# Optimization experiments

Measured on AMD Instinct MI355X. Metric: run time of the kernel, lower is better.

The kernel has to match this reference:

```python
import jax, jax.numpy as jnp
import numpy as np

NEG_SLOPE = 0.2  # PyG GATConv default negative_slope


def gat_conv(x, src, dst, W, a_src, a_dst, b, n_nodes):
    # x: [N, Cin]; W: [H, Cin, Cout]; a_src/a_dst: [H, Cout]; b: [Cout]
    xh = jnp.einsum('ni,hio->nho', x, W)                 # [N, H, Cout]
    al_s = jnp.einsum('nho,ho->nh', xh, a_src)           # [N, H]
    al_d = jnp.einsum('nho,ho->nh', xh, a_dst)           # [N, H]
    e = jax.nn.leaky_relu(al_s[src] + al_d[dst], NEG_SLOPE)  # [E, H]
    # softmax over incoming edges of each dst node (self-loops guarantee >=1 edge)
    m = jax.ops.segment_max(e, dst, num_segments=n_nodes)
    ex = jnp.exp(e - m[dst])
    den = jax.ops.segment_sum(ex, dst, num_segments=n_nodes)
    alpha = ex / den[dst]                                # [E, H]
    msg = alpha[:, :, None] * xh[src]                    # [E, H, Cout]
    out = jax.ops.segment_sum(msg, dst, num_segments=n_nodes)  # [N, H, Cout]
    return out.mean(axis=1) + b                          # concat=False -> head mean


def setup_inputs() -> dict:
    key = jax.random.key(0)
    ks = jax.random.split(key, 16)
    N, E, C, H = 20000, 320000, 128, 4
    s = 1.0 / np.sqrt(C)
    inp = {
        'x': jax.random.normal(ks[0], (N, C), dtype=jnp.float32),
        'edge_index': jax.random.randint(ks[1], (2, E), 0, N, dtype=jnp.int64),
    }
    for i, name in enumerate(['1', '2', 'r']):
        k0, k1, k2 = jax.random.split(ks[2 + i], 3)
        inp['W' + name] = jax.random.normal(k0, (H, C, C), dtype=jnp.float32) * s
        inp['as' + name] = jax.random.normal(k1, (H, C), dtype=jnp.float32) * s
        inp['ad' + name] = jax.random.normal(k2, (H, C), dtype=jnp.float32) * s
        inp['b' + name] = jnp.zeros((C,), dtype=jnp.float32)
    return inp


def reference(x, edge_index, W1, as1, ad1, b1, W2, as2, ad2, b2, Wr, asr, adr, br):
    n = x.shape[0]
    loop = jnp.arange(n, dtype=edge_index.dtype)
    src = jnp.concatenate([edge_index[0], loop])  # PyG add_self_loops=True
    dst = jnp.concatenate([edge_index[1], loop])
    h = gat_conv(x, src, dst, W1, as1, ad1, b1, n)
    h = gat_conv(h, src, dst, W2, as2, ad2, b2, n)
    res = gat_conv(x, src, dst, Wr, asr, adr, br, n)
    return h + res
```

## Files before the change

kernel.cpp:

```cpp
#include <hip/hip_runtime.h>
#include <math.h>

#define C 128

typedef unsigned short u16;
typedef __attribute__((ext_vector_type(8))) short short8;
typedef __attribute__((ext_vector_type(4))) float f32x4;
typedef __attribute__((ext_vector_type(4))) u16 u16x4;

__device__ __forceinline__ float b2f(u16 u) {
    union { unsigned i; float f; } x; x.i = (unsigned)u << 16; return x.f;
}
__device__ __forceinline__ u16 f2b(float f) {
    union { float f; unsigned i; } x; x.f = f;
    unsigned r = x.i + 0x7FFFu + ((x.i >> 16) & 1u);
    return (u16)(r >> 16);
}
__device__ __forceinline__ float lrelu(float x) { return x > 0.f ? x : 0.2f * x; }


__global__ void hist_kernel(const int* __restrict__ ei, int E, int N,
                            int* __restrict__ count) {
    int total = E + N;
    for (int e = blockIdx.x * blockDim.x + threadIdx.x; e < total;
         e += gridDim.x * blockDim.x) {
        int d = (e < E) ? ei[E + e] : (e - E);
        if ((unsigned)d < (unsigned)N) atomicAdd(&count[d], 1);
    }
}

__global__ __launch_bounds__(1024) void scan_kernel(const int* __restrict__ count,
                                                    int* __restrict__ offs,
                                                    int* __restrict__ cursor, int N) {
    int tid = threadIdx.x, lane = tid & 63, wid = tid >> 6;
    int CH = (N + 1023) >> 10;
    int base = tid * CH;
    int s = 0;
    for (int j = 0; j < CH; ++j) {
        int i = base + j;
        if (i < N) s += count[i];
    }
    int own = s;
    #pragma unroll
    for (int d = 1; d < 64; d <<= 1) {
        int v = __shfl_up(s, d);
        if (lane >= d) s += v;
    }
    __shared__ int wtot[16];
    if (lane == 63) wtot[wid] = s;
    __syncthreads();
    if (tid < 16) {
        int t = wtot[tid];
        int u = t;
        #pragma unroll
        for (int d = 1; d < 16; d <<= 1) {
            int v = __shfl_up(u, d);
            if (tid >= d) u += v;
        }
        wtot[tid] = u - t;
        if (tid == 15) offs[N] = u;
    }
    __syncthreads();
    int run = wtot[wid] + s - own;
    for (int j = 0; j < CH; ++j) {
        int i = base + j;
        if (i < N) {
            offs[i] = run;
            cursor[i] = run;
            run += count[i];
        }
    }
}

__global__ void scatter_kernel(const int* __restrict__ ei, int E, int N,
                               int* __restrict__ cursor, int* __restrict__ srcs,
                               int* __restrict__ dsts) {
    int total = E + N;
    for (int e = blockIdx.x * blockDim.x + threadIdx.x; e < total;
         e += gridDim.x * blockDim.x) {
        int sNode, d;
        if (e < E) { sNode = ei[e]; d = ei[E + e]; }
        else       { sNode = e - E; d = sNode; }
        if ((unsigned)d < (unsigned)N && (unsigned)sNode < (unsigned)N) {
            int pos = atomicAdd(&cursor[d], 1);
            srcs[pos] = sNode;
            dsts[pos] = d;
        }
    }
}

__global__ __launch_bounds__(128) void cvt_w_kernel(const float* __restrict__ W1,
                                                    const float* __restrict__ Wr,
                                                    const float* __restrict__ W2,
                                                    u16* __restrict__ Wc) {
    int b = blockIdx.x;
    int l = b >> 7, o = b & 127;
    const float* W = (l == 0) ? W1 : (l == 1) ? Wr : W2;
    int i = threadIdx.x;
    u16* dst = Wc + ((size_t)l * C + o) * 512;
    #pragma unroll
    for (int h = 0; h < 4; ++h) {
        dst[h * C + i] = f2b(0.25f * W[((size_t)h * C + i) * C + o]);
    }
}


__global__ __launch_bounds__(256) void wvec_kernel(const float* __restrict__ W1,
                                                   const float* __restrict__ as1,
                                                   const float* __restrict__ ad1,
                                                   const float* __restrict__ Wr,
                                                   const float* __restrict__ asr,
                                                   const float* __restrict__ adr,
                                                   const float* __restrict__ W2,
                                                   const float* __restrict__ as2,
                                                   const float* __restrict__ ad2,
                                                   u16* __restrict__ vsdA,
                                                   u16* __restrict__ vsdB) {
    int slot = blockIdx.x;
    const float* W  = (slot < 4) ? W1 : (slot < 8) ? Wr : W2;
    const float* s_ = (slot < 4) ? as1 : (slot < 8) ? asr : as2;
    const float* d_ = (slot < 4) ? ad1 : (slot < 8) ? adr : ad2;
    int h = slot & 3;
    int wave = threadIdx.x >> 6, lane = threadIdx.x & 63;
    int rbase = blockIdx.y * 32 + wave * 8;
    float as0 = s_[h * C + lane], as1v = s_[h * C + 64 + lane];
    float ad0 = d_[h * C + lane], ad1v = d_[h * C + 64 + lane];
    #pragma unroll
    for (int j = 0; j < 8; ++j) {
        int i = rbase + j;
        const float* Wrow = W + ((size_t)h * C + i) * C;
        float w0 = Wrow[lane], w1 = Wrow[64 + lane];
        float ps = w0 * as0 + w1 * as1v;
        float pd = w0 * ad0 + w1 * ad1v;
        #pragma unroll
        for (int m = 32; m; m >>= 1) {
            ps += __shfl_xor(ps, m);
            pd += __shfl_xor(pd, m);
        }
        if (lane == 0) {
            if (slot < 8) {
                vsdA[slot * C + i] = f2b(ps);
                vsdA[(8 + slot) * C + i] = f2b(pd);
            } else {
                vsdB[(slot - 8) * C + i] = f2b(ps);
                vsdB[(4 + (slot - 8)) * C + i] = f2b(pd);
            }
        }
    }
}


__global__ __launch_bounds__(256) void alA_kernel(const float* __restrict__ x,
                                                  const u16* __restrict__ vsd,
                                                  u16* __restrict__ xb,
                                                  float* __restrict__ als,
                                                  float* __restrict__ ald, int N) {
    int wave = threadIdx.x >> 6, lane = threadIdx.x & 63;
    int rowBase = blockIdx.x * 64 + wave * 16;
    int r = rowBase + (lane & 15);
    int rl = r < N ? r : N - 1;
    int kg = (lane >> 4) * 8;

    short8 a[4];
    #pragma unroll
    for (int t = 0; t < 4; ++t) {
        const float* xp = x + (size_t)rl * C + t * 32 + kg;
        float4 f0 = *(const float4*)xp;
        float4 f1 = *(const float4*)(xp + 4);
        short8 s;
        s[0] = f2b(f0.x); s[1] = f2b(f0.y); s[2] = f2b(f0.z); s[3] = f2b(f0.w);
        s[4] = f2b(f1.x); s[5] = f2b(f1.y); s[6] = f2b(f1.z); s[7] = f2b(f1.w);
        a[t] = s;
        if (r < N) *(short8*)(xb + (size_t)r * C + t * 32 + kg) = s;
    }
    f32x4 acc = {0.f, 0.f, 0.f, 0.f};
    int col = lane & 15;
    #pragma unroll
    for (int t = 0; t < 4; ++t) {
        short8 b = *(const short8*)(vsd + (size_t)col * C + t * 32 + kg);
        acc = __builtin_amdgcn_mfma_f32_16x16x32_bf16(a[t], b, acc, 0, 0, 0);
    }
    #pragma unroll
    for (int j = 0; j < 4; ++j) {
        int rr = rowBase + (lane >> 4) * 4 + j;
        if (rr < N) {
            if (col < 8) als[rr * 8 + col] = acc[j];
            else ald[rr * 8 + (col - 8)] = acc[j];
        }
    }
}


__global__ __launch_bounds__(256) void alB_kernel(const u16* __restrict__ in,
                                                  const u16* __restrict__ vsd,
                                                  float* __restrict__ als,
                                                  float* __restrict__ ald, int N) {
    int wave = threadIdx.x >> 6, lane = threadIdx.x & 63;
    int rowBase = blockIdx.x * 64 + wave * 16;
    int r = rowBase + (lane & 15);
    int rl = r < N ? r : N - 1;
    int kg = (lane >> 4) * 8;

    f32x4 acc = {0.f, 0.f, 0.f, 0.f};
    int col = lane & 15;
    #pragma unroll
    for (int t = 0; t < 4; ++t) {
        short8 a = *(const short8*)(in + (size_t)rl * C + t * 32 + kg);
        short8 b = *(const short8*)(vsd + (size_t)col * C + t * 32 + kg);
        acc = __builtin_amdgcn_mfma_f32_16x16x32_bf16(a, b, acc, 0, 0, 0);
    }
    #pragma unroll
    for (int j = 0; j < 4; ++j) {
        int rr = rowBase + (lane >> 4) * 4 + j;
        if (rr < N && col < 8) {
            if (col < 4) als[rr * 4 + col] = acc[j];
            else ald[rr * 4 + (col - 4)] = acc[j];
        }
    }
}


template <int NH>
__global__ __launch_bounds__(256) void ew_kernel(const float* __restrict__ als,
                                                 const float* __restrict__ ald,
                                                 const int* __restrict__ srcs,
                                                 const int* __restrict__ dsts,
                                                 float* __restrict__ wout, int ET) {
    int i = blockIdx.x * blockDim.x + threadIdx.x;
    if (i >= ET) return;
    int s = srcs[i], d = dsts[i];
    const float* as_ = als + (size_t)s * NH;
    const float* ad_ = ald + (size_t)d * NH;
    float* wo = wout + (size_t)i * NH;
    #pragma unroll
    for (int h = 0; h < NH; ++h) {
        wo[h] = __expf(lrelu(as_[h] + ad_[h]));
    }
}


template <int NH>
__global__ __launch_bounds__(256) void den_kernel(const float* __restrict__ wgt,
                                                  const int* __restrict__ offs,
                                                  float* __restrict__ den, int N) {
    int idx = blockIdx.x * blockDim.x + threadIdx.x;
    int node = idx / NH, h = idx % NH;
    if (node >= N) return;
    int beg = offs[node], end = offs[node + 1];
    float s = 0.f;
    for (int i = beg; i < end; ++i) s += wgt[(size_t)i * NH + h];
    den[idx] = s;
}


template <int NH>
__global__ __launch_bounds__(256) void aggx_kernel(const u16* __restrict__ xsrc,
                                                   const float* __restrict__ wgt,
                                                   const float* __restrict__ den,
                                                   const int* __restrict__ offs,
                                                   const int* __restrict__ srcs,
                                                   u16* __restrict__ dest, int N) {
    constexpr int NHG = NH / 2;
    int node = blockIdx.x * 4 + (threadIdx.x >> 6);
    int lane = threadIdx.x & 63;
    if (node >= N) return;
    int g = lane >> 5;
    int c0 = (lane & 31) * 4;
    int beg = offs[node], end = offs[node + 1];

    float inv[NHG];
    #pragma unroll
    for (int j = 0; j < NHG; ++j) {
        inv[j] = 1.f / den[(size_t)node * NH + g * NHG + j];
    }

    float acc[NHG][4] = {};
    int i = beg;
    for (; i + 8 <= end; i += 8) {
        int s[8];
        #pragma unroll
        for (int e = 0; e < 8; ++e) s[e] = srcs[i + e];
        u16x4 v[8];
        #pragma unroll
        for (int e = 0; e < 8; ++e) {
            v[e] = *(const u16x4*)(xsrc + (size_t)s[e] * C + c0);
        }
        float wv[8][NHG];
        #pragma unroll
        for (int e = 0; e < 8; ++e) {
            if constexpr (NHG == 4) {
                float4 wq = *(const float4*)(wgt + (size_t)(i + e) * NH + g * NHG);
                wv[e][0] = wq.x; wv[e][1] = wq.y; wv[e][2] = wq.z; wv[e][3] = wq.w;
            } else {
                float2 wq = *(const float2*)(wgt + (size_t)(i + e) * NH + g * NHG);
                wv[e][0] = wq.x; wv[e][1] = wq.y;
            }
        }
        #pragma unroll
        for (int e = 0; e < 8; ++e) {
            float f[4];
            #pragma unroll
            for (int j = 0; j < 4; ++j) f[j] = b2f(v[e][j]);
            #pragma unroll
            for (int j2 = 0; j2 < NHG; ++j2) {
                #pragma unroll
                for (int j = 0; j < 4; ++j) acc[j2][j] += wv[e][j2] * f[j];
            }
        }
    }
    for (; i < end; ++i) {
        int s0 = srcs[i];
        u16x4 v0 = *(const u16x4*)(xsrc + (size_t)s0 * C + c0);
        float w0[NHG];
        #pragma unroll
        for (int j2 = 0; j2 < NHG; ++j2) {
            w0[j2] = wgt[(size_t)i * NH + g * NHG + j2];
        }
        float f[4];
        #pragma unroll
        for (int j = 0; j < 4; ++j) f[j] = b2f(v0[j]);
        #pragma unroll
        for (int j2 = 0; j2 < NHG; ++j2) {
            #pragma unroll
            for (int j = 0; j < 4; ++j) acc[j2][j] += w0[j2] * f[j];
        }
    }

    #pragma unroll
    for (int j2 = 0; j2 < NHG; ++j2) {
        int h = g * NHG + j2;
        u16x4 o = {f2b(acc[j2][0] * inv[j2]), f2b(acc[j2][1] * inv[j2]),
                   f2b(acc[j2][2] * inv[j2]), f2b(acc[j2][3] * inv[j2])};
        *(u16x4*)(dest + (size_t)node * (NH * C) + h * C + c0) = o;
    }
}


__global__ __launch_bounds__(256) void gemm2ab_kernel(const u16* __restrict__ agg,
                                                      const u16* __restrict__ Wc,
                                                      const float* __restrict__ b1,
                                                      const float* __restrict__ br,
                                                      u16* __restrict__ h1b,
                                                      float* __restrict__ outf, int N) {
    int part = blockIdx.y;
    const u16* A = agg + part * 512;
    const u16* W = Wc + (size_t)part * C * 512;
    const float* bias = part ? br : b1;

    int wave = threadIdx.x >> 6, lane = threadIdx.x & 63;
    int rowBase = blockIdx.x * 64 + wave * 16;
    int r = rowBase + (lane & 15);
    int rl = r < N ? r : N - 1;
    int kg = (lane >> 4) * 8;

    const short8* ap = (const short8*)(A + (size_t)rl * 1024 + kg);
    const short8* bp = (const short8*)(W + (size_t)(lane & 15) * 512 + kg);

    f32x4 acc[8];
    #pragma unroll
    for (int t = 0; t < 8; ++t) acc[t] = (f32x4){0.f, 0.f, 0.f, 0.f};

    #pragma unroll
    for (int kk = 0; kk < 16; ++kk) {
        short8 a = ap[kk * 4];
        #pragma unroll
        for (int t = 0; t < 8; ++t) {
            acc[t] = __builtin_amdgcn_mfma_f32_16x16x32_bf16(
                a, bp[(size_t)t * 16 * 64 + kk * 4], acc[t], 0, 0, 0);
        }
    }

    int prow = rowBase + (lane >> 4) * 4;
    #pragma unroll
    for (int t = 0; t < 8; ++t) {
        int col = t * 16 + (lane & 15);
        float bcol = bias[col];
        #pragma unroll
        for (int j = 0; j < 4; ++j) {
            int rr = prow + j;
            if (rr < N) {
                float v = acc[t][j] + bcol;
                if (part == 0) h1b[(size_t)rr * C + col] = f2b(v);
                else outf[(size_t)rr * C + col] = v;
            }
        }
    }
}


__global__ __launch_bounds__(256) void gemm2c_kernel(const u16* __restrict__ A,
                                                     const u16* __restrict__ Wc,
                                                     const float* __restrict__ bias,
                                                     float* __restrict__ outf, int N) {
    int wave = threadIdx.x >> 6, lane = threadIdx.x & 63;
    int rowBase = blockIdx.x * 64 + wave * 16;
    int r = rowBase + (lane & 15);
    int rl = r < N ? r : N - 1;
    int kg = (lane >> 4) * 8;

    const short8* ap = (const short8*)(A + (size_t)rl * 512 + kg);
    const short8* bp = (const short8*)(Wc + (size_t)(lane & 15) * 512 + kg);

    f32x4 acc[8];
    #pragma unroll
    for (int t = 0; t < 8; ++t) acc[t] = (f32x4){0.f, 0.f, 0.f, 0.f};

    #pragma unroll
    for (int kk = 0; kk < 16; ++kk) {
        short8 a = ap[kk * 4];
        #pragma unroll
        for (int t = 0; t < 8; ++t) {
            acc[t] = __builtin_amdgcn_mfma_f32_16x16x32_bf16(
                a, bp[(size_t)t * 16 * 64 + kk * 4], acc[t], 0, 0, 0);
        }
    }

    int prow = rowBase + (lane >> 4) * 4;
    #pragma unroll
    for (int t = 0; t < 8; ++t) {
        int col = t * 16 + (lane & 15);
        float bcol = bias[col];
        #pragma unroll
        for (int j = 0; j < 4; ++j) {
            int rr = prow + j;
            if (rr < N) outf[(size_t)rr * C + col] += acc[t][j] + bcol;
        }
    }
}


extern "C" void kernel_launch(void* const* d_in, const int* in_sizes, int n_in,
                              void* d_out, int out_size, void* d_ws, size_t ws_size,
                              hipStream_t stream) {
    const float* x = (const float*)d_in[0];
    const int* ei = (const int*)d_in[1];
    const float* W1 = (const float*)d_in[2];
    const float* as1 = (const float*)d_in[3];
    const float* ad1 = (const float*)d_in[4];
    const float* b1 = (const float*)d_in[5];
    const float* W2 = (const float*)d_in[6];
    const float* as2 = (const float*)d_in[7];
    const float* ad2 = (const float*)d_in[8];
    const float* b2 = (const float*)d_in[9];
    const float* Wr = (const float*)d_in[10];
    const float* asr = (const float*)d_in[11];
    const float* adr = (const float*)d_in[12];
    const float* br = (const float*)d_in[13];

    int N = in_sizes[0] / C;
    int E = in_sizes[1] / 2;
    int ET = E + N;

    size_t sz_xb    = (size_t)N * C * 2;
    size_t sz_h1b   = (size_t)N * C * 2;
    size_t sz_aggA  = (size_t)N * 1024 * 2;
    size_t sz_aggB  = (size_t)N * 512 * 2;
    size_t sz_wc    = (size_t)3 * C * 512 * 2;
    size_t sz_vsd   = (size_t)16 * C * 2;
    size_t sz_al8   = (size_t)N * 8 * 4;
    size_t sz_count = (size_t)N * 4;
    size_t sz_den8  = (size_t)N * 8 * 4;
    size_t sz_den4  = (size_t)N * 4 * 4;
    size_t sz_offs  = (size_t)(N + 4) * 4;
    size_t sz_srcs  = (size_t)ET * 4;
    size_t sz_w     = (size_t)ET * 8 * 4;
    size_t required = sz_xb + sz_h1b + sz_aggA + sz_aggB + sz_wc + 2 * sz_vsd +
                      2 * sz_al8 + sz_count + sz_den8 + sz_den4 + sz_count +
                      sz_offs + 2 * sz_srcs + sz_w;
    if (ws_size < required) return;

    char* w = (char*)d_ws;
    u16* xb = (u16*)w;        w += sz_xb;
    u16* h1b = (u16*)w;       w += sz_h1b;
    u16* aggA = (u16*)w;      w += sz_aggA;
    u16* aggB = (u16*)w;      w += sz_aggB;
    u16* Wc = (u16*)w;        w += sz_wc;
    u16* vsdA = (u16*)w;      w += sz_vsd;
    u16* vsdB = (u16*)w;      w += sz_vsd;
    float* als = (float*)w;   w += sz_al8;
    float* ald = (float*)w;   w += sz_al8;
    int* count = (int*)w;     w += sz_count;
    float* den8 = (float*)w;  w += sz_den8;
    float* den4 = (float*)w;  w += sz_den4;
    int* cursor = (int*)w;    w += sz_count;
    int* offs = (int*)w;      w += sz_offs;
    int* srcs = (int*)w;      w += sz_srcs;
    int* dsts = (int*)w;      w += sz_srcs;
    float* wgt = (float*)w;   w += sz_w;
    float* out = (float*)d_out;

    const u16* Wc2 = Wc + (size_t)2 * C * 512;

    hipMemsetAsync(count, 0, sz_count, stream);
    hist_kernel<<<512, 256, 0, stream>>>(ei, E, N, count);
    scan_kernel<<<1, 1024, 0, stream>>>(count, offs, cursor, N);
    scatter_kernel<<<512, 256, 0, stream>>>(ei, E, N, cursor, srcs, dsts);

    cvt_w_kernel<<<384, 128, 0, stream>>>(W1, Wr, W2, Wc);
    wvec_kernel<<<dim3(12, 4), 256, 0, stream>>>(W1, as1, ad1, Wr, asr, adr,
                                                 W2, as2, ad2, vsdA, vsdB);

    int nwb = (N + 3) / 4;
    int neb = (ET + 255) / 256;
    int gx = (N + 63) / 64;
    int nd8 = (N * 8 + 255) / 256;
    int nd4 = (N * 4 + 255) / 256;

    alA_kernel<<<gx, 256, 0, stream>>>(x, vsdA, xb, als, ald, N);
    ew_kernel<8><<<neb, 256, 0, stream>>>(als, ald, srcs, dsts, wgt, ET);
    den_kernel<8><<<nd8, 256, 0, stream>>>(wgt, offs, den8, N);
    aggx_kernel<8><<<nwb, 256, 0, stream>>>(xb, wgt, den8, offs, srcs, aggA, N);
    gemm2ab_kernel<<<dim3(gx, 2), 256, 0, stream>>>(aggA, Wc, b1, br, h1b, out, N);

    alB_kernel<<<gx, 256, 0, stream>>>(h1b, vsdB, als, ald, N);
    ew_kernel<4><<<neb, 256, 0, stream>>>(als, ald, srcs, dsts, wgt, ET);
    den_kernel<4><<<nd4, 256, 0, stream>>>(wgt, offs, den4, N);
    aggx_kernel<4><<<nwb, 256, 0, stream>>>(h1b, wgt, den4, offs, srcs, aggB, N);
    gemm2c_kernel<<<gx, 256, 0, stream>>>(aggB, Wc2, b2, out, N);
}
```

Measured before the change: 375.8 us.

## Pre-swizzle bf16 weights into MFMA fragment order and double rows per wave

The weight-conversion kernel now writes bf16 weights already arranged in per-lane MFMA B-fragment order, so each lane loads its B operand as one contiguous 16-byte read that coalesces across the wave instead of a strided one. Both output GEMM kernels also process two 16-row tiles per wave (128 rows per block), reusing each loaded B fragment for two MFMAs. This halves weight traffic per row, at the cost of more accumulator registers and half as many blocks.

```diff
diff --git a/kernel.cpp b/kernel.cpp
--- a/kernel.cpp
+++ b/kernel.cpp
@@ -89,19 +89,27 @@
     }
 }
 
-__global__ __launch_bounds__(128) void cvt_w_kernel(const float* __restrict__ W1,
+
+__global__ __launch_bounds__(256) void cvt_w_kernel(const float* __restrict__ W1,
                                                     const float* __restrict__ Wr,
                                                     const float* __restrict__ W2,
-                                                    u16* __restrict__ Wc) {
-    int b = blockIdx.x;
-    int l = b >> 7, o = b & 127;
+                                                    u16* __restrict__ Wf) {
+    int idx = blockIdx.x * 256 + threadIdx.x;
+    int lane = idx & 63;
+    int kk = (idx >> 6) & 15;
+    int t = (idx >> 10) & 7;
+    int l = idx >> 13;
+    if (l >= 3) return;
     const float* W = (l == 0) ? W1 : (l == 1) ? Wr : W2;
-    int i = threadIdx.x;
-    u16* dst = Wc + ((size_t)l * C + o) * 512;
-    #pragma unroll
-    for (int h = 0; h < 4; ++h) {
-        dst[h * C + i] = f2b(0.25f * W[((size_t)h * C + i) * C + o]);
-    }
+    int o = t * 16 + (lane & 15);
+    int bk = kk * 32 + (lane >> 4) * 8;
+    int h = bk >> 7, i0 = bk & 127;
+    short8 v;
+    #pragma unroll
+    for (int j = 0; j < 8; ++j) {
+        v[j] = (short)f2b(0.25f * W[((size_t)h * C + i0 + j) * C + o]);
+    }
+    *(short8*)(Wf + (size_t)idx * 8) = v;
 }
 
 
@@ -337,93 +345,112 @@
 
 
 __global__ __launch_bounds__(256) void gemm2ab_kernel(const u16* __restrict__ agg,
-                                                      const u16* __restrict__ Wc,
+                                                      const u16* __restrict__ Wf,
                                                       const float* __restrict__ b1,
                                                       const float* __restrict__ br,
                                                       u16* __restrict__ h1b,
                                                       float* __restrict__ outf, int N) {
     int part = blockIdx.y;
-    const u16* A = agg + part * 512;
-    const u16* W = Wc + (size_t)part * C * 512;
     const float* bias = part ? br : b1;
-
     int wave = threadIdx.x >> 6, lane = threadIdx.x & 63;
-    int rowBase = blockIdx.x * 64 + wave * 16;
-    int r = rowBase + (lane & 15);
-    int rl = r < N ? r : N - 1;
-    int kg = (lane >> 4) * 8;
-
-    const short8* ap = (const short8*)(A + (size_t)rl * 1024 + kg);
-    const short8* bp = (const short8*)(W + (size_t)(lane & 15) * 512 + kg);
-
-    f32x4 acc[8];
-    #pragma unroll
-    for (int t = 0; t < 8; ++t) acc[t] = (f32x4){0.f, 0.f, 0.f, 0.f};
+    int rowBase = blockIdx.x * 128 + wave * 32;
+    int p = lane & 15, q = lane >> 4;
+    int r0 = rowBase + p, r1 = rowBase + 16 + p;
+    int rl0 = r0 < N ? r0 : N - 1;
+    int rl1 = r1 < N ? r1 : N - 1;
+    int kg = q * 8;
+
+    const short8* ap0 = (const short8*)(agg + (size_t)rl0 * 1024 + part * 512 + kg);
+    const short8* ap1 = (const short8*)(agg + (size_t)rl1 * 1024 + part * 512 + kg);
+    const u16* wb = Wf + (size_t)part * 65536 + lane * 8;
+
+    f32x4 acc0[8], acc1[8];
+    #pragma unroll
+    for (int t = 0; t < 8; ++t) {
+        acc0[t] = (f32x4){0.f, 0.f, 0.f, 0.f};
+        acc1[t] = (f32x4){0.f, 0.f, 0.f, 0.f};
+    }
 
     #pragma unroll
     for (int kk = 0; kk < 16; ++kk) {
-        short8 a = ap[kk * 4];
+        short8 a0 = ap0[kk * 4];
+        short8 a1 = ap1[kk * 4];
         #pragma unroll
         for (int t = 0; t < 8; ++t) {
-            acc[t] = __builtin_amdgcn_mfma_f32_16x16x32_bf16(
-                a, bp[(size_t)t * 16 * 64 + kk * 4], acc[t], 0, 0, 0);
-        }
-    }
-
-    int prow = rowBase + (lane >> 4) * 4;
+            short8 b = *(const short8*)(wb + (size_t)(t * 16 + kk) * 512);
+            acc0[t] = __builtin_amdgcn_mfma_f32_16x16x32_bf16(a0, b, acc0[t], 0, 0, 0);
+            acc1[t] = __builtin_amdgcn_mfma_f32_16x16x32_bf16(a1, b, acc1[t], 0, 0, 0);
+        }
+    }
+
     #pragma unroll
     for (int t = 0; t < 8; ++t) {
-        int col = t * 16 + (lane & 15);
+        int col = t * 16 + p;
         float bcol = bias[col];
         #pragma unroll
         for (int j = 0; j < 4; ++j) {
-            int rr = prow + j;
-            if (rr < N) {
-                float v = acc[t][j] + bcol;
-                if (part == 0) h1b[(size_t)rr * C + col] = f2b(v);
-                else outf[(size_t)rr * C + col] = v;
+            int rr0 = rowBase + q * 4 + j;
+            int rr1 = rowBase + 16 + q * 4 + j;
+            if (rr0 < N) {
+                float v = acc0[t][j] + bcol;
+                if (part == 0) h1b[(size_t)rr0 * C + col] = f2b(v);
+                else outf[(size_t)rr0 * C + col] = v;
             }
+            if (rr1 < N) {
+                float v = acc1[t][j] + bcol;
+                if (part == 0) h1b[(size_t)rr1 * C + col] = f2b(v);
+                else outf[(size_t)rr1 * C + col] = v;
+            }
         }
     }
 }
 
 
 __global__ __launch_bounds__(256) void gemm2c_kernel(const u16* __restrict__ A,
-                                                     const u16* __restrict__ Wc,
+                                                     const u16* __restrict__ Wf,
                                                      const float* __restrict__ bias,
                                                      float* __restrict__ outf, int N) {
     int wave = threadIdx.x >> 6, lane = threadIdx.x & 63;
-    int rowBase = blockIdx.x * 64 + wave * 16;
-    int r = rowBase + (lane & 15);
-    int rl = r < N ? r : N - 1;
-    int kg = (lane >> 4) * 8;
-
-    const short8* ap = (const short8*)(A + (size_t)rl * 512 + kg);
-    const short8* bp = (const short8*)(Wc + (size_t)(lane & 15) * 512 + kg);
-
-    f32x4 acc[8];
-    #pragma unroll
-    for (int t = 0; t < 8; ++t) acc[t] = (f32x4){0.f, 0.f, 0.f, 0.f};
+    int rowBase = blockIdx.x * 128 + wave * 32;
+    int p = lane & 15, q = lane >> 4;
+    int r0 = rowBase + p, r1 = rowBase + 16 + p;
+    int rl0 = r0 < N ? r0 : N - 1;
+    int rl1 = r1 < N ? r1 : N - 1;
+    int kg = q * 8;
+
+    const short8* ap0 = (const short8*)(A + (size_t)rl0 * 512 + kg);
+    const short8* ap1 = (const short8*)(A + (size_t)rl1 * 512 + kg);
+    const u16* wb = Wf + (size_t)2 * 65536 + lane * 8;
+
+    f32x4 acc0[8], acc1[8];
+    #pragma unroll
+    for (int t = 0; t < 8; ++t) {
+        acc0[t] = (f32x4){0.f, 0.f, 0.f, 0.f};
+        acc1[t] = (f32x4){0.f, 0.f, 0.f, 0.f};
+    }
 
     #pragma unroll
     for (int kk = 0; kk < 16; ++kk) {
-        short8 a = ap[kk * 4];
+        short8 a0 = ap0[kk * 4];
+        short8 a1 = ap1[kk * 4];
         #pragma unroll
         for (int t = 0; t < 8; ++t) {
-            acc[t] = __builtin_amdgcn_mfma_f32_16x16x32_bf16(
-                a, bp[(size_t)t * 16 * 64 + kk * 4], acc[t], 0, 0, 0);
-        }
-    }
-
-    int prow = rowBase + (lane >> 4) * 4;
+            short8 b = *(const short8*)(wb + (size_t)(t * 16 + kk) * 512);
+            acc0[t] = __builtin_amdgcn_mfma_f32_16x16x32_bf16(a0, b, acc0[t], 0, 0, 0);
+            acc1[t] = __builtin_amdgcn_mfma_f32_16x16x32_bf16(a1, b, acc1[t], 0, 0, 0);
+        }
+    }
+
     #pragma unroll
     for (int t = 0; t < 8; ++t) {
-        int col = t * 16 + (lane & 15);
+        int col = t * 16 + p;
         float bcol = bias[col];
         #pragma unroll
         for (int j = 0; j < 4; ++j) {
-            int rr = prow + j;
-            if (rr < N) outf[(size_t)rr * C + col] += acc[t][j] + bcol;
+            int rr0 = rowBase + q * 4 + j;
+            int rr1 = rowBase + 16 + q * 4 + j;
+            if (rr0 < N) outf[(size_t)rr0 * C + col] += acc0[t][j] + bcol;
+            if (rr1 < N) outf[(size_t)rr1 * C + col] += acc1[t][j] + bcol;
         }
     }
 }
@@ -474,7 +501,7 @@
     u16* h1b = (u16*)w;       w += sz_h1b;
     u16* aggA = (u16*)w;      w += sz_aggA;
     u16* aggB = (u16*)w;      w += sz_aggB;
-    u16* Wc = (u16*)w;        w += sz_wc;
+    u16* Wf = (u16*)w;        w += sz_wc;
     u16* vsdA = (u16*)w;      w += sz_vsd;
     u16* vsdB = (u16*)w;      w += sz_vsd;
     float* als = (float*)w;   w += sz_al8;
@@ -489,20 +516,19 @@
     float* wgt = (float*)w;   w += sz_w;
     float* out = (float*)d_out;
 
-    const u16* Wc2 = Wc + (size_t)2 * C * 512;
-
     hipMemsetAsync(count, 0, sz_count, stream);
     hist_kernel<<<512, 256, 0, stream>>>(ei, E, N, count);
     scan_kernel<<<1, 1024, 0, stream>>>(count, offs, cursor, N);
     scatter_kernel<<<512, 256, 0, stream>>>(ei, E, N, cursor, srcs, dsts);
 
-    cvt_w_kernel<<<384, 128, 0, stream>>>(W1, Wr, W2, Wc);
+    cvt_w_kernel<<<96, 256, 0, stream>>>(W1, Wr, W2, Wf);
     wvec_kernel<<<dim3(12, 4), 256, 0, stream>>>(W1, as1, ad1, Wr, asr, adr,
                                                  W2, as2, ad2, vsdA, vsdB);
 
     int nwb = (N + 3) / 4;
     int neb = (ET + 255) / 256;
     int gx = (N + 63) / 64;
+    int gx2 = (N + 127) / 128;
     int nd8 = (N * 8 + 255) / 256;
     int nd4 = (N * 4 + 255) / 256;
 
@@ -510,11 +536,11 @@
     ew_kernel<8><<<neb, 256, 0, stream>>>(als, ald, srcs, dsts, wgt, ET);
     den_kernel<8><<<nd8, 256, 0, stream>>>(wgt, offs, den8, N);
     aggx_kernel<8><<<nwb, 256, 0, stream>>>(xb, wgt, den8, offs, srcs, aggA, N);
-    gemm2ab_kernel<<<dim3(gx, 2), 256, 0, stream>>>(aggA, Wc, b1, br, h1b, out, N);
+    gemm2ab_kernel<<<dim3(gx2, 2), 256, 0, stream>>>(aggA, Wf, b1, br, h1b, out, N);
 
     alB_kernel<<<gx, 256, 0, stream>>>(h1b, vsdB, als, ald, N);
     ew_kernel<4><<<neb, 256, 0, stream>>>(als, ald, srcs, dsts, wgt, ET);
     den_kernel<4><<<nd4, 256, 0, stream>>>(wgt, offs, den4, N);
     aggx_kernel<4><<<nwb, 256, 0, stream>>>(h1b, wgt, den4, offs, srcs, aggB, N);
-    gemm2c_kernel<<<gx, 256, 0, stream>>>(aggB, Wc2, b2, out, N);
-}
+    gemm2c_kernel<<<gx2, 256, 0, stream>>>(aggB, Wf, b2, out, N);
+}
```

Result: faster. 365.9 us (-2.6%).
